# Kernel optimization log

Measured on AMD Instinct MI355X. Metric: run time of the kernel, lower is better.

## Reference

```python
import jax, jax.numpy as jnp
import numpy as np

L = 4          # GAT_LAYERS
HEADS = 4      # N_HEADS
H = 64         # transformer hidden dim
DH = H // HEADS
FIN = 32       # NODE_EMBED_SIZE
A = 15         # gats.num_actions (readout size)
OBS = 1500     # flattened obs dim
HS = 512       # hidden_size (policy FC)
NOUT = 15      # num_outputs
VH = 128       # VALUE_HIDDENS
B = 128        # batch of graphs
N = 1000       # nodes per map graph
TOT = B * N
DEG = 4
E = TOT * DEG


def _lin(key, fan_in, shape):
    return jax.random.normal(key, shape, jnp.float32) * (1.0 / np.sqrt(fan_in))


def setup_inputs() -> dict:
    key = jax.random.key(0)
    ks = jax.random.split(key, 30)
    node_feats = jax.random.normal(ks[0], (TOT, FIN), jnp.float32)
    obs = jax.random.normal(ks[1], (B, OBS), jnp.float32)
    # batched-graph edges: endpoints stay within each graph (DGL batch semantics)
    off = (jnp.arange(B) * N)[:, None]
    edge_src = (jax.random.randint(ks[2], (B, N * DEG), 0, N) + off).reshape(-1).astype(jnp.int32)
    edge_dst = (jax.random.randint(ks[3], (B, N * DEG), 0, N) + off).reshape(-1).astype(jnp.int32)
    agent_nodes = (jax.random.randint(ks[4], (B,), 0, N) + jnp.arange(B) * N).astype(jnp.int32)
    p = {
        'W_in': _lin(ks[5], FIN, (FIN, H)),
        'Wq': _lin(ks[6], H, (L, H, H)), 'Wk': _lin(ks[7], H, (L, H, H)),
        'Wv': _lin(ks[8], H, (L, H, H)), 'Wo': _lin(ks[9], H, (L, H, H)),
        'ln1_g': jnp.ones((L, H), jnp.float32), 'ln1_b': jnp.zeros((L, H), jnp.float32),
        'W1': _lin(ks[10], H, (L, H, 2 * H)), 'b1': jnp.zeros((L, 2 * H), jnp.float32),
        'W2': _lin(ks[11], 2 * H, (L, 2 * H, H)), 'b2': jnp.zeros((L, H), jnp.float32),
        'ln2_g': jnp.ones((L, H), jnp.float32), 'ln2_b': jnp.zeros((L, H), jnp.float32),
        'Wr': _lin(ks[12], H, (H, A)), 'br': jnp.zeros((A,), jnp.float32),
        'Wp1': _lin(ks[13], A + OBS, (A + OBS, HS)), 'bp1': jnp.zeros((HS,), jnp.float32),
        'Wp2': _lin(ks[14], HS, (HS, HS)), 'bp2': jnp.zeros((HS,), jnp.float32),
        'Wlog': _lin(ks[15], HS, (HS, NOUT)), 'blog': jnp.zeros((NOUT,), jnp.float32),
        'Wv1': _lin(ks[16], OBS, (OBS, VH)), 'bv1': jnp.zeros((VH,), jnp.float32),
        'Wv2': _lin(ks[17], VH, (VH, VH)), 'bv2': jnp.zeros((VH,), jnp.float32),
        'Wvo': _lin(ks[18], VH, (VH, 1)), 'bvo': jnp.zeros((1,), jnp.float32),
    }
    return dict(node_feats=node_feats, obs=obs, edge_src=edge_src, edge_dst=edge_dst,
                agent_nodes=agent_nodes, **p)


def _layernorm(x, g, b):
    m = x.mean(-1, keepdims=True)
    v = ((x - m) ** 2).mean(-1, keepdims=True)
    return (x - m) * jax.lax.rsqrt(v + 1e-5) * g + b


def reference(node_feats, obs, edge_src, edge_dst, agent_nodes, W_in, Wq, Wk, Wv, Wo,
              ln1_g, ln1_b, W1, b1, W2, b2, ln2_g, ln2_b, Wr, br,
              Wp1, bp1, Wp2, bp2, Wlog, blog, Wv1, bv1, Wv2, bv2, Wvo, bvo):
    n = node_feats.shape[0]
    x = node_feats @ W_in                                   # [n, H]
    inv_sqrt_dh = np.float32(1.0 / np.sqrt(DH))
    for l in range(L):
        q = (x @ Wq[l]).reshape(n, HEADS, DH)
        k = (x @ Wk[l]).reshape(n, HEADS, DH)
        v = (x @ Wv[l]).reshape(n, HEADS, DH)
        # per-edge attention scores, softmax over incoming edges of each dst node
        s = jnp.sum(q[edge_dst] * k[edge_src], axis=-1) * inv_sqrt_dh   # [E, HEADS]
        m = jax.ops.segment_max(s, edge_dst, num_segments=n)            # [n, HEADS]
        w = jnp.exp(s - m[edge_dst])
        denom = jax.ops.segment_sum(w, edge_dst, num_segments=n)        # [n, HEADS]
        agg = jax.ops.segment_sum(w[:, :, None] * v[edge_src], edge_dst, num_segments=n)
        attn = (agg / (denom[:, :, None] + 1e-9)).reshape(n, H) @ Wo[l]
        x = _layernorm(x + attn, ln1_g[l], ln1_b[l])
        h = jax.nn.relu(x @ W1[l] + b1[l]) @ W2[l] + b2[l]
        x = _layernorm(x + h, ln2_g[l], ln2_b[l])
    gat_out = x[agent_nodes] @ Wr + br                      # [B, A] per-agent action features
    feat = jnp.tanh(jnp.concatenate([gat_out, obs], axis=1) @ Wp1 + bp1)
    feat = jnp.tanh(feat @ Wp2 + bp2)
    logits = feat @ Wlog + blog                             # [B, NOUT]
    vh = jnp.tanh(obs @ Wv1 + bv1)
    vh = jnp.tanh(vh @ Wv2 + bv2)
    value = (vh @ Wvo + bvo)[:, 0]                          # [B]
    return logits, value
```

## Files before the change

### kernel.cpp

```cpp
#include <hip/hip_runtime.h>
#include <hip/hip_bf16.h>
#include <cstdint>
#include <cstddef>

#define DEV static __device__ __forceinline__

constexpr int GRAPHS = 128;
constexpr int NPG    = 1000;
constexpr int EPG    = 4000;
constexpr int TOTN   = GRAPHS * NPG;
constexpr int TOTE   = GRAPHS * EPG;
constexpr int HD     = 64;
constexpr int OBSD   = 1500;
constexpr int AD     = 15;

typedef __attribute__((ext_vector_type(8))) short bf16x8;
typedef __attribute__((ext_vector_type(4))) float f32x4;

DEV unsigned short f2b(float f){
  unsigned u = __float_as_uint(f);
  return (unsigned short)((u + 0x7fffu + ((u >> 16) & 1u)) >> 16);
}
DEV float b2f(unsigned short s){ return __uint_as_float((unsigned)s << 16); }

DEV void fma4(float4& a, float s, const float4 w){
  a.x = fmaf(s, w.x, a.x); a.y = fmaf(s, w.y, a.y);
  a.z = fmaf(s, w.z, a.z); a.w = fmaf(s, w.w, a.w);
}

DEV ushort4 pack4(float4 v){
  ushort4 r; r.x=f2b(v.x); r.y=f2b(v.y); r.z=f2b(v.z); r.w=f2b(v.w); return r;
}

__global__ __launch_bounds__(256) void k_wprep(const float* __restrict__ Wq,
    const float* __restrict__ Wk, const float* __restrict__ Wv,
    const float* __restrict__ Wo, const float* __restrict__ W1,
    const float* __restrict__ W2, unsigned short* __restrict__ wpack){
  int e = blockIdx.x*256 + threadIdx.x;
  int l = e >> 15;
  int r = e & 32767;
  float val;
  if (r < 12288){
    int c = r >> 6, k = r & 63;
    val = (c < 64)  ? Wq[l*4096 + k*64 + c]
        : (c < 128) ? Wk[l*4096 + k*64 + (c-64)]
                    : Wv[l*4096 + k*64 + (c-128)];
  } else if (r < 16384){
    int i = r - 12288; int c = i >> 6, k = i & 63;
    val = Wo[l*4096 + k*64 + c];
  } else if (r < 24576){
    int i = r - 16384; int c = i >> 6, k = i & 63;
    val = W1[l*8192 + k*128 + c];
  } else {
    int i = r - 24576; int c = i >> 7, k = i & 127;
    val = W2[l*8192 + k*64 + c];
  }
  wpack[e] = f2b(val);
}

__global__ __launch_bounds__(256) void k_zero(int* __restrict__ cnt){
  cnt[blockIdx.x*256 + threadIdx.x] = 0;
}

__global__ __launch_bounds__(256) void k_hist(const int* __restrict__ edst,
                                              int* __restrict__ cnt){
  int e = blockIdx.x*256 + threadIdx.x;
  atomicAdd(&cnt[edst[e]], 1);
}

__global__ __launch_bounds__(1024) void k_scan(const int* __restrict__ cnt,
    int* __restrict__ rstart, int* __restrict__ cursor){
  __shared__ int s[1024];
  const int g = blockIdx.x, tid = threadIdx.x;
  int v = (tid < NPG) ? cnt[g*NPG + tid] : 0;
  s[tid] = v;
  __syncthreads();
  #pragma unroll
  for (int off=1; off<1024; off<<=1){
    int t = (tid >= off) ? s[tid-off] : 0;
    __syncthreads();
    s[tid] += t;
    __syncthreads();
  }
  if (tid < NPG){
    int r = g*EPG + (s[tid] - v);
    rstart[g*NPG+tid] = r;
    cursor[g*NPG+tid] = r;
  }
}

__global__ __launch_bounds__(256) void k_scatter(const int* __restrict__ esrc,
    const int* __restrict__ edst, int* __restrict__ cursor,
    int* __restrict__ esorted){
  int e = blockIdx.x*256 + threadIdx.x;
  int pos = atomicAdd(&cursor[edst[e]], 1);
  esorted[pos] = esrc[e];
}

__global__ __launch_bounds__(256) void k_in(const float* __restrict__ nf,
                                            const float* __restrict__ Win,
                                            unsigned short* __restrict__ xb){
  __shared__ float  s_nf[256*36];
  __shared__ float4 s_w[512];
  const int tid = threadIdx.x;
  const int node0 = blockIdx.x * 256;
  const float4* W4 = (const float4*)Win;
  s_w[tid] = W4[tid]; s_w[tid+256] = W4[tid+256];
  const float4* nf4 = (const float4*)nf;
  float4* snf4 = (float4*)s_nf;
  #pragma unroll
  for (int r=0;r<8;r++){
    int i = tid + 256*r; int n = i>>3, k4 = i&7;
    snf4[n*9 + k4] = nf4[(size_t)(node0+n)*8 + k4];
  }
  __syncthreads();
  const int ng = tid>>2, cg = tid&3;
  float4 acc[4][4];
  #pragma unroll
  for (int i=0;i<4;i++){ acc[i][0]=make_float4(0,0,0,0); acc[i][1]=make_float4(0,0,0,0);
                         acc[i][2]=make_float4(0,0,0,0); acc[i][3]=make_float4(0,0,0,0); }
  #pragma unroll 4
  for (int k=0;k<32;k++){
    float nv[4];
    #pragma unroll
    for (int i=0;i<4;i++) nv[i] = s_nf[(ng + 64*i)*36 + k];
    float4 w[4];
    #pragma unroll
    for (int j=0;j<4;j++) w[j] = s_w[k*16 + cg*4 + j];
    #pragma unroll
    for (int i=0;i<4;i++){
      #pragma unroll
      for (int j=0;j<4;j++) fma4(acc[i][j], nv[i], w[j]);
    }
  }
  ushort4* xb4 = (ushort4*)xb;
  #pragma unroll
  for (int i=0;i<4;i++){
    size_t nidx = (size_t)(node0 + ng + 64*i) * 16;
    #pragma unroll
    for (int j=0;j<4;j++) xb4[nidx + cg*4 + j] = pack4(acc[i][j]);
  }
}

__global__ __launch_bounds__(256) void k_qkv_m(const unsigned short* __restrict__ xb,
    const unsigned short* __restrict__ wqkvT,
    unsigned short* __restrict__ qkv){
  __shared__ short s_w[192*72];
  __shared__ short s_st[4][16*104];
  const int tid = threadIdx.x;
  const int node0 = blockIdx.x * 256;
  {
    const unsigned* src = (const unsigned*)wqkvT;
    unsigned* dst = (unsigned*)s_w;
    #pragma unroll
    for (int r=0;r<24;r++){
      int j = tid + 256*r;
      int c = j >> 5, kk = j & 31;
      dst[c*36 + kk] = src[j];
    }
  }
  __syncthreads();
  const int lane = tid & 63, wave = tid >> 6;
  const int m = lane & 15, quad = lane >> 4;
  const int rowbase = node0 + wave*64;
  bf16x8 af[4][2];
  #pragma unroll
  for (int rt=0;rt<4;rt++){
    const unsigned short* xp = xb + (size_t)(rowbase + rt*16 + m)*64 + quad*8;
    af[rt][0] = *(const bf16x8*)xp;
    af[rt][1] = *(const bf16x8*)(xp + 32);
  }
  short* st = s_st[wave];
  #pragma unroll
  for (int rt=0;rt<4;rt++){
    #pragma unroll
    for (int half=0; half<2; half++){
      #pragma unroll
      for (int c6=0;c6<6;c6++){
        int ct = half*6 + c6;
        bf16x8 b0 = *(const bf16x8*)&s_w[(ct*16+m)*72 + quad*8];
        bf16x8 b1 = *(const bf16x8*)&s_w[(ct*16+m)*72 + 32 + quad*8];
        f32x4 acc = {0.f,0.f,0.f,0.f};
        acc = __builtin_amdgcn_mfma_f32_16x16x32_bf16(af[rt][0], b0, acc, 0,0,0);
        acc = __builtin_amdgcn_mfma_f32_16x16x32_bf16(af[rt][1], b1, acc, 0,0,0);
        #pragma unroll
        for (int i=0;i<4;i++)
          st[(quad*4+i)*104 + c6*16 + m] = (short)f2b(acc[i]);
      }
      #pragma unroll
      for (int j=0;j<3;j++){
        int flat = (j*64 + lane)*8;
        int r = flat / 96, c = flat % 96;
        bf16x8 v = *(const bf16x8*)&st[r*104 + c];
        *(bf16x8*)(qkv + (size_t)(rowbase + rt*16 + r)*192 + half*96 + c) = v;
      }
    }
  }
}

__global__ __launch_bounds__(256) void k_edge2(const unsigned short* __restrict__ qkv,
    const int* __restrict__ rstart, const int* __restrict__ cnt,
    const int* __restrict__ esorted, unsigned short* __restrict__ attn_in){
  const int tid = threadIdx.x;
  const int wb = (blockIdx.x & 7)*1000 + (blockIdx.x >> 3);
  const int lane = tid & 63;
  const int sub  = lane >> 4;
  const int dg   = lane & 15;
  const int wave = tid >> 6;
  const int node = wb*16 + wave*4 + sub;
  ushort4 qu = *(const ushort4*)(qkv + (size_t)node*192 + dg*4);
  float q0 = b2f(qu.x), q1 = b2f(qu.y), q2 = b2f(qu.z), q3 = b2f(qu.w);
  const int rs = rstart[node];
  const int n  = cnt[node];
  const int nn = min(n, 16);
  int myidx = (dg < nn) ? esorted[rs + dg] : node;
  const int lbase = lane & 48;
  float a0=0.f, a1=0.f, a2=0.f, a3=0.f, den=0.f;
  ushort4 kA, vA, kB, vB;
  if (nn > 0){
    int s0 = __shfl(myidx, lbase);
    kA = *(const ushort4*)(qkv + (size_t)s0*192 + 64 + dg*4);
    vA = *(const ushort4*)(qkv + (size_t)s0*192 + 128 + dg*4);
  }
  if (nn > 1){
    int s1 = __shfl(myidx, lbase + 1);
    kB = *(const ushort4*)(qkv + (size_t)s1*192 + 64 + dg*4);
    vB = *(const ushort4*)(qkv + (size_t)s1*192 + 128 + dg*4);
  }
  for (int i=0;i<nn;i++){
    ushort4 ck = kA, cv = vA;
    kA = kB; vA = vB;
    if (i+2 < nn){
      int s2 = __shfl(myidx, lbase + i + 2);
      kB = *(const ushort4*)(qkv + (size_t)s2*192 + 64 + dg*4);
      vB = *(const ushort4*)(qkv + (size_t)s2*192 + 128 + dg*4);
    }
    float p = q0*b2f(ck.x) + q1*b2f(ck.y) + q2*b2f(ck.z) + q3*b2f(ck.w);
    p += __shfl_xor(p, 1);
    p += __shfl_xor(p, 2);
    float w = __expf(p * 0.25f);
    den += w;
    a0 = fmaf(w, b2f(cv.x), a0);
    a1 = fmaf(w, b2f(cv.y), a1);
    a2 = fmaf(w, b2f(cv.z), a2);
    a3 = fmaf(w, b2f(cv.w), a3);
  }
  for (int i=16;i<n;i++){
    int src = esorted[rs + i];
    ushort4 ku = *(const ushort4*)(qkv + (size_t)src*192 + 64 + dg*4);
    ushort4 vu = *(const ushort4*)(qkv + (size_t)src*192 + 128 + dg*4);
    float p = q0*b2f(ku.x) + q1*b2f(ku.y) + q2*b2f(ku.z) + q3*b2f(ku.w);
    p += __shfl_xor(p, 1);
    p += __shfl_xor(p, 2);
    float w = __expf(p * 0.25f);
    den += w;
    a0 = fmaf(w, b2f(vu.x), a0);
    a1 = fmaf(w, b2f(vu.y), a1);
    a2 = fmaf(w, b2f(vu.z), a2);
    a3 = fmaf(w, b2f(vu.w), a3);
  }
  float inv = 1.0f/(den + 1e-9f);
  ushort4 o;
  o.x = f2b(a0*inv); o.y = f2b(a1*inv); o.z = f2b(a2*inv); o.w = f2b(a3*inv);
  ((ushort4*)attn_in)[(size_t)node*16 + dg] = o;
}

__global__ __launch_bounds__(256) void k_attn_ffn(
    const unsigned short* __restrict__ attn_in,
    unsigned short* __restrict__ xb,
    const unsigned short* __restrict__ woT,
    const unsigned short* __restrict__ w1T, const float* __restrict__ b1_l,
    const unsigned short* __restrict__ w2T, const float* __restrict__ b2_l,
    const float* __restrict__ l1g, const float* __restrict__ l1b,
    const float* __restrict__ l2g, const float* __restrict__ l2b,
    const unsigned short* __restrict__ wqkvT,
    unsigned short* __restrict__ qkv){
  __shared__ short s_w1[128*72];
  __shared__ short s_w2[64*136];
  __shared__ short s_st[4][16*136];
  const int tid = threadIdx.x;
  const int node0 = blockIdx.x*256;
  {
    const unsigned* src = (const unsigned*)w1T;
    unsigned* dst = (unsigned*)s_w1;
    #pragma unroll
    for (int r=0;r<16;r++){
      int j = tid + 256*r;
      int c = j >> 5, kk = j & 31;
      dst[c*36 + kk] = src[j];
    }
  }
  {
    const unsigned* src = (const unsigned*)w2T;
    unsigned* dst = (unsigned*)s_w2;
    #pragma unroll
    for (int r=0;r<16;r++){
      int j = tid + 256*r;
      int c = j >> 6, kk = j & 63;
      dst[c*68 + kk] = src[j];
    }
  }
  const int lane = tid&63, wave = tid>>6;
  const int m = lane&15, quad = lane>>4;
  const int rowbase = node0 + wave*64;
  bf16x8 wo[4][2];
  #pragma unroll
  for (int ct=0;ct<4;ct++){
    wo[ct][0] = *(const bf16x8*)&woT[(ct*16+m)*64 + quad*8];
    wo[ct][1] = *(const bf16x8*)&woT[(ct*16+m)*64 + 32 + quad*8];
  }
  float g1[4], bb1[4], g2[4], bb2[4], b2v[4];
  #pragma unroll
  for (int ct=0;ct<4;ct++){
    g1[ct]=l1g[ct*16+m]; bb1[ct]=l1b[ct*16+m];
    g2[ct]=l2g[ct*16+m]; bb2[ct]=l2b[ct*16+m];
    b2v[ct]=b2_l[ct*16+m];
  }
  float b1v[8];
  #pragma unroll
  for (int ct=0;ct<8;ct++) b1v[ct]=b1_l[ct*16+m];
  bf16x8 af[4][2];
  #pragma unroll
  for (int rt=0;rt<4;rt++){
    const unsigned short* ap = attn_in + (size_t)(rowbase + rt*16 + m)*64 + quad*8;
    af[rt][0] = *(const bf16x8*)ap;
    af[rt][1] = *(const bf16x8*)(ap + 32);
  }
  __syncthreads();
  short* st = s_st[wave];
  #pragma unroll
  for (int rt=0;rt<4;rt++){
    f32x4 acc[4];
    #pragma unroll
    for (int ct=0;ct<4;ct++){
      f32x4 z = {0.f,0.f,0.f,0.f};
      z = __builtin_amdgcn_mfma_f32_16x16x32_bf16(af[rt][0], wo[ct][0], z, 0,0,0);
      z = __builtin_amdgcn_mfma_f32_16x16x32_bf16(af[rt][1], wo[ct][1], z, 0,0,0);
      acc[ct] = z;
    }
    float x1v[4][4];
    #pragma unroll
    for (int i=0;i<4;i++){
      size_t row = (size_t)(rowbase + rt*16 + quad*4 + i)*64;
      float v0 = acc[0][i] + b2f(xb[row + m]);
      float v1 = acc[1][i] + b2f(xb[row + 16 + m]);
      float v2 = acc[2][i] + b2f(xb[row + 32 + m]);
      float v3 = acc[3][i] + b2f(xb[row + 48 + m]);
      float sm = v0+v1+v2+v3;
      float sq = v0*v0+v1*v1+v2*v2+v3*v3;
      #pragma unroll
      for (int mk=1; mk<16; mk<<=1){ sm += __shfl_xor(sm, mk); sq += __shfl_xor(sq, mk); }
      float mean = sm*0.015625f;
      float var  = sq*0.015625f - mean*mean;
      float rs   = rsqrtf(var + 1e-5f);
      x1v[i][0] = (v0-mean)*rs*g1[0]+bb1[0];
      x1v[i][1] = (v1-mean)*rs*g1[1]+bb1[1];
      x1v[i][2] = (v2-mean)*rs*g1[2]+bb1[2];
      x1v[i][3] = (v3-mean)*rs*g1[3]+bb1[3];
      int rl = quad*4 + i;
      st[rl*136 + m]      = (short)f2b(x1v[i][0]);
      st[rl*136 + 16 + m] = (short)f2b(x1v[i][1]);
      st[rl*136 + 32 + m] = (short)f2b(x1v[i][2]);
      st[rl*136 + 48 + m] = (short)f2b(x1v[i][3]);
    }
    bf16x8 x10 = *(const bf16x8*)&st[m*136 + quad*8];
    bf16x8 x11 = *(const bf16x8*)&st[m*136 + 32 + quad*8];
    #pragma unroll
    for (int ct=0;ct<8;ct++){
      bf16x8 b0 = *(const bf16x8*)&s_w1[(ct*16+m)*72 + quad*8];
      bf16x8 b1 = *(const bf16x8*)&s_w1[(ct*16+m)*72 + 32 + quad*8];
      f32x4 z = {0.f,0.f,0.f,0.f};
      z = __builtin_amdgcn_mfma_f32_16x16x32_bf16(x10, b0, z, 0,0,0);
      z = __builtin_amdgcn_mfma_f32_16x16x32_bf16(x11, b1, z, 0,0,0);
      #pragma unroll
      for (int i=0;i<4;i++)
        st[(quad*4+i)*136 + ct*16 + m] = (short)f2b(fmaxf(z[i]+b1v[ct], 0.f));
    }
    bf16x8 h0 = *(const bf16x8*)&st[m*136 + quad*8];
    bf16x8 h1 = *(const bf16x8*)&st[m*136 + 32 + quad*8];
    bf16x8 h2 = *(const bf16x8*)&st[m*136 + 64 + quad*8];
    bf16x8 h3 = *(const bf16x8*)&st[m*136 + 96 + quad*8];
    f32x4 acc2[4];
    #pragma unroll
    for (int ct=0;ct<4;ct++){
      f32x4 z = {0.f,0.f,0.f,0.f};
      z = __builtin_amdgcn_mfma_f32_16x16x32_bf16(h0, *(const bf16x8*)&s_w2[(ct*16+m)*136 + quad*8],      z, 0,0,0);
      z = __builtin_amdgcn_mfma_f32_16x16x32_bf16(h1, *(const bf16x8*)&s_w2[(ct*16+m)*136 + 32 + quad*8], z, 0,0,0);
      z = __builtin_amdgcn_mfma_f32_16x16x32_bf16(h2, *(const bf16x8*)&s_w2[(ct*16+m)*136 + 64 + quad*8], z, 0,0,0);
      z = __builtin_amdgcn_mfma_f32_16x16x32_bf16(h3, *(const bf16x8*)&s_w2[(ct*16+m)*136 + 96 + quad*8], z, 0,0,0);
      acc2[ct] = z;
    }
    #pragma unroll
    for (int i=0;i<4;i++){
      float v0 = acc2[0][i] + b2v[0] + x1v[i][0];
      float v1 = acc2[1][i] + b2v[1] + x1v[i][1];
      float v2 = acc2[2][i] + b2v[2] + x1v[i][2];
      float v3 = acc2[3][i] + b2v[3] + x1v[i][3];
      float sm = v0+v1+v2+v3;
      float sq = v0*v0+v1*v1+v2*v2+v3*v3;
      #pragma unroll
      for (int mk=1; mk<16; mk<<=1){ sm += __shfl_xor(sm, mk); sq += __shfl_xor(sq, mk); }
      float mean = sm*0.015625f;
      float var  = sq*0.015625f - mean*mean;
      float rs   = rsqrtf(var + 1e-5f);
      int rl = quad*4 + i;
      st[rl*136 + m]      = (short)f2b((v0-mean)*rs*g2[0]+bb2[0]);
      st[rl*136 + 16 + m] = (short)f2b((v1-mean)*rs*g2[1]+bb2[1]);
      st[rl*136 + 32 + m] = (short)f2b((v2-mean)*rs*g2[2]+bb2[2]);
      st[rl*136 + 48 + m] = (short)f2b((v3-mean)*rs*g2[3]+bb2[3]);
    }
    #pragma unroll
    for (int j=0;j<2;j++){
      int flat = (j*64 + lane)*8;
      int r = flat >> 6, c = flat & 63;
      bf16x8 v = *(const bf16x8*)&st[r*136 + c];
      *(bf16x8*)(xb + (size_t)(rowbase + rt*16 + r)*64 + c) = v;
    }
    if (wqkvT){
      bf16x8 x20 = *(const bf16x8*)&st[m*136 + quad*8];
      bf16x8 x21 = *(const bf16x8*)&st[m*136 + 32 + quad*8];
      #pragma unroll
      for (int half=0; half<2; half++){
        #pragma unroll
        for (int c6=0;c6<6;c6++){
          int ct = half*6 + c6;
          bf16x8 b0 = *(const bf16x8*)&wqkvT[(ct*16+m)*64 + quad*8];
          bf16x8 b1 = *(const bf16x8*)&wqkvT[(ct*16+m)*64 + 32 + quad*8];
          f32x4 z = {0.f,0.f,0.f,0.f};
          z = __builtin_amdgcn_mfma_f32_16x16x32_bf16(x20, b0, z, 0,0,0);
          z = __builtin_amdgcn_mfma_f32_16x16x32_bf16(x21, b1, z, 0,0,0);
          #pragma unroll
          for (int i=0;i<4;i++)
            st[(quad*4+i)*136 + c6*16 + m] = (short)f2b(z[i]);
        }
        #pragma unroll
        for (int j=0;j<3;j++){
          int flat = (j*64 + lane)*8;
          int r = flat / 96, c = flat % 96;
          bf16x8 v = *(const bf16x8*)&st[r*136 + c];
          *(bf16x8*)(qkv + (size_t)(rowbase + rt*16 + r)*192 + half*96 + c) = v;
        }
      }
    }
  }
}

__global__ __launch_bounds__(512) void k_fc1(const unsigned short* __restrict__ xb,
    const float* __restrict__ obs, const int* __restrict__ agents,
    const float* __restrict__ Wr, const float* __restrict__ br,
    const float* __restrict__ Wp1, float* __restrict__ part1){
  constexpr int ROWS=2, COLS=256, CH=384, K=1515, N=512;
  const int chunk = 379;
  __shared__ float s_a[ROWS*CH];
  const int tid = threadIdx.x;
  const int ct = blockIdx.x, rg = blockIdx.y, ks = blockIdx.z;
  const int k0 = ks * chunk;
  const int len = min(K - k0, chunk);
  const int row0 = rg * ROWS;
  #pragma unroll
  for (int rr=0; rr<ROWS; rr++)
    for (int i=tid; i<len; i+=512){
      int k = k0 + i;
      if (k >= AD) s_a[rr*CH + i] = obs[(size_t)(row0+rr)*OBSD + (k-AD)];
    }
  if (ks==0 && tid < ROWS*AD){
    int rr = tid/AD, c = tid%AD;
    int b = row0 + rr;
    const unsigned short* xa = xb + (size_t)agents[b]*HD;
    float a = br[c];
    #pragma unroll 8
    for (int k=0;k<HD;k++) a = fmaf(b2f(xa[k]), Wr[k*AD + c], a);
    s_a[rr*CH + c] = a;
  }
  __syncthreads();
  const int r = tid / COLS, c = tid % COLS;
  const float* wp = Wp1 + (size_t)k0*N + ct*COLS + c;
  const float* ap = s_a + r*CH;
  float acc = 0.f;
  #pragma unroll 8
  for (int k=0;k<len;k++) acc = fmaf(ap[k], wp[(size_t)k*N], acc);
  part1[((size_t)ks*128 + row0 + r)*N + ct*COLS + c] = acc;
}

__global__ __launch_bounds__(512) void k_fc2(const float* __restrict__ part1,
    const float* __restrict__ bp1, const float* __restrict__ Wp2,
    float* __restrict__ part2){
  constexpr int ROWS=2, COLS=256, CH=256, N=512;
  __shared__ float s_a[ROWS*CH];
  const int tid = threadIdx.x;
  const int ct = blockIdx.x, rg = blockIdx.y, ks = blockIdx.z;
  const int k0 = ks * CH;
  const int row0 = rg * ROWS;
  #pragma unroll
  for (int rr=0; rr<ROWS; rr++)
    for (int i=tid; i<CH; i+=512){
      int k = k0 + i;
      float s = bp1[k];
      #pragma unroll
      for (int j=0;j<4;j++) s += part1[((size_t)j*128 + row0+rr)*512 + k];
      s_a[rr*CH + i] = tanhf(s);
    }
  __syncthreads();
  const int r = tid / COLS, c = tid % COLS;
  const float* wp = Wp2 + (size_t)k0*N + ct*COLS + c;
  const float* ap = s_a + r*CH;
  float acc = 0.f;
  #pragma unroll 8
  for (int k=0;k<CH;k++) acc = fmaf(ap[k], wp[(size_t)k*N], acc);
  part2[((size_t)ks*128 + row0 + r)*N + ct*COLS + c] = acc;
}

__global__ __launch_bounds__(256) void k_logits(const float* __restrict__ part2,
    const float* __restrict__ bp2, const float* __restrict__ Wlog,
    const float* __restrict__ blog, float* __restrict__ out){
  __shared__ float s_f[512];
  __shared__ float s_p[16*AD];
  const int b = blockIdx.x, tid = threadIdx.x;
  for (int i=tid;i<512;i+=256){
    float s = bp2[i] + part2[(size_t)b*512 + i] + part2[(size_t)(128+b)*512 + i];
    s_f[i] = tanhf(s);
  }
  __syncthreads();
  if (tid < 240){
    int c = tid % AD, kc = tid / AD;
    float a = 0.f;
    #pragma unroll 8
    for (int j=0;j<32;j++){ int k = kc*32 + j; a = fmaf(s_f[k], Wlog[k*AD + c], a); }
    s_p[tid] = a;
  }
  __syncthreads();
  if (tid < AD){
    float a = blog[tid];
    #pragma unroll
    for (int kc=0;kc<16;kc++) a += s_p[kc*AD + tid];
    out[(size_t)b*AD + tid] = a;
  }
}

template<int ROWS, int COLS, int CH, int KS, int N>
__global__ __launch_bounds__(ROWS*COLS) void k_gemm_part(
    const float* __restrict__ A, int lda, int K,
    const float* __restrict__ W, float* __restrict__ part){
  constexpr int BT = ROWS*COLS;
  __shared__ float s_a[ROWS*CH];
  const int tid = threadIdx.x;
  const int ct = blockIdx.x, rg = blockIdx.y, ks = blockIdx.z;
  const int chunk = (K + KS - 1) / KS;
  const int k0 = ks * chunk;
  const int len = min(K - k0, chunk);
  const int row0 = rg * ROWS;
  #pragma unroll
  for (int rr=0; rr<ROWS; rr++)
    for (int i=tid; i<len; i+=BT)
      s_a[rr*CH + i] = A[(size_t)(row0+rr)*lda + k0 + i];
  __syncthreads();
  const int r = tid / COLS, c = tid % COLS;
  const float* wp = W + (size_t)k0*N + ct*COLS + c;
  const float* ap = s_a + r*CH;
  float acc = 0.f;
  #pragma unroll 8
  for (int k=0;k<len;k++) acc = fmaf(ap[k], wp[(size_t)k*N], acc);
  part[((size_t)ks*128 + row0 + r)*N + ct*COLS + c] = acc;
}

__global__ __launch_bounds__(128) void k_vfin(const float* __restrict__ partv,
    const float* __restrict__ bv1, const float* __restrict__ Wv2,
    const float* __restrict__ bv2, const float* __restrict__ Wvo,
    const float* __restrict__ bvo, float* __restrict__ out){
  __shared__ float s_v[128];
  __shared__ float s_r[128];
  const int b = blockIdx.x, tid = threadIdx.x;
  {
    float s = bv1[tid];
    #pragma unroll
    for (int j=0;j<8;j++) s += partv[((size_t)j*128 + b)*128 + tid];
    s_v[tid] = tanhf(s);
  }
  __syncthreads();
  float a = bv2[tid];
  #pragma unroll 8
  for (int k=0;k<128;k++) a = fmaf(s_v[k], Wv2[k*128 + tid], a);
  s_r[tid] = tanhf(a) * Wvo[tid];
  __syncthreads();
  if (tid < 64){
    float v = s_r[tid] + s_r[tid+64];
    #pragma unroll
    for (int m=32;m>=1;m>>=1) v += __shfl_xor(v, m);
    if (tid==0) out[GRAPHS*AD + b] = v + bvo[0];
  }
}

extern "C" void kernel_launch(void* const* d_in, const int* in_sizes, int n_in,
                              void* d_out, int out_size, void* d_ws, size_t ws_size,
                              hipStream_t stream) {
  (void)in_sizes; (void)n_in; (void)out_size; (void)ws_size;
  const float* nf     = (const float*)d_in[0];
  const float* obs    = (const float*)d_in[1];
  const int*   esrc   = (const int*)d_in[2];
  const int*   edst   = (const int*)d_in[3];
  const int*   agents = (const int*)d_in[4];
  const float* Win    = (const float*)d_in[5];
  const float* Wq     = (const float*)d_in[6];
  const float* Wk     = (const float*)d_in[7];
  const float* Wv     = (const float*)d_in[8];
  const float* Wo     = (const float*)d_in[9];
  const float* ln1g   = (const float*)d_in[10];
  const float* ln1b   = (const float*)d_in[11];
  const float* W1     = (const float*)d_in[12];
  const float* b1     = (const float*)d_in[13];
  const float* W2     = (const float*)d_in[14];
  const float* b2     = (const float*)d_in[15];
  const float* ln2g   = (const float*)d_in[16];
  const float* ln2b   = (const float*)d_in[17];
  const float* Wr     = (const float*)d_in[18];
  const float* br     = (const float*)d_in[19];
  const float* Wp1    = (const float*)d_in[20];
  const float* bp1    = (const float*)d_in[21];
  const float* Wp2    = (const float*)d_in[22];
  const float* bp2    = (const float*)d_in[23];
  const float* Wlog   = (const float*)d_in[24];
  const float* blog   = (const float*)d_in[25];
  const float* Wv1    = (const float*)d_in[26];
  const float* bv1    = (const float*)d_in[27];
  const float* Wv2    = (const float*)d_in[28];
  const float* bv2    = (const float*)d_in[29];
  const float* Wvo    = (const float*)d_in[30];
  const float* bvo    = (const float*)d_in[31];
  float* out = (float*)d_out;

  unsigned short* xb      = (unsigned short*)d_ws;
  unsigned short* qkv     = xb + (size_t)TOTN*HD;
  unsigned short* attn_in = qkv + (size_t)TOTN*192;
  unsigned short* wpack   = attn_in + (size_t)TOTN*HD;
  int* cnt     = (int*)(wpack + 131072);
  int* rstart  = cnt + TOTN;
  int* cursor  = rstart + TOTN;
  int* esorted = cursor + TOTN;
  float* part1 = (float*)(esorted + TOTE);
  float* part2 = part1 + 4*128*512;
  float* partv = part2 + 2*128*512;

  k_wprep  <<<512, 256, 0, stream>>>(Wq, Wk, Wv, Wo, W1, W2, wpack);
  k_zero   <<<TOTN/256, 256, 0, stream>>>(cnt);
  k_hist   <<<TOTE/256, 256, 0, stream>>>(edst, cnt);
  k_scan   <<<GRAPHS, 1024, 0, stream>>>(cnt, rstart, cursor);
  k_scatter<<<TOTE/256, 256, 0, stream>>>(esrc, edst, cursor, esorted);

  k_in<<<TOTN/256, 256, 0, stream>>>(nf, Win, xb);
  k_qkv_m<<<TOTN/256, 256, 0, stream>>>(xb, wpack, qkv);
  for (int l=0; l<4; l++){
    const unsigned short* wl = wpack + l*32768;
    const unsigned short* wqkv_next = (l<3) ? (wpack + (l+1)*32768) : nullptr;
    k_edge2   <<<TOTN/16, 256, 0, stream>>>(qkv, rstart, cnt, esorted, attn_in);
    k_attn_ffn<<<TOTN/256, 256, 0, stream>>>(attn_in, xb,
                                             wl + 12288,
                                             wl + 16384, b1 + l*128,
                                             wl + 24576, b2 + l*64,
                                             ln1g + l*64, ln1b + l*64,
                                             ln2g + l*64, ln2b + l*64,
                                             wqkv_next, qkv);
  }
  k_fc1   <<<dim3(2,64,4), 512, 0, stream>>>(xb, obs, agents, Wr, br, Wp1, part1);
  k_fc2   <<<dim3(2,64,2), 512, 0, stream>>>(part1, bp1, Wp2, part2);
  k_logits<<<GRAPHS, 256, 0, stream>>>(part2, bp2, Wlog, blog, out);
  k_gemm_part<4,128,192,8,128><<<dim3(1,32,8), 512, 0, stream>>>(obs, 1500, 1500, Wv1, partv);
  k_vfin  <<<GRAPHS, 128, 0, stream>>>(partv, bv1, Wv2, bv2, Wvo, bvo, out);
}
```

Before: 483.4 us.

## Shrink attn-FFN blocks to one wave and read FFN weights from global

Result: slower. 658.8 us (+36.3%).

```diff
diff --git a/kernel.cpp b/kernel.cpp
--- a/kernel.cpp
+++ b/kernel.cpp
@@ -265,7 +265,7 @@
   ((ushort4*)attn_in)[(size_t)node*16 + dg] = o;
 }
 
-__global__ __launch_bounds__(256) void k_attn_ffn(
+__global__ __launch_bounds__(64, 4) void k_attn_ffn(
     const unsigned short* __restrict__ attn_in,
     unsigned short* __restrict__ xb,
     const unsigned short* __restrict__ woT,
@@ -275,34 +275,10 @@
     const float* __restrict__ l2g, const float* __restrict__ l2b,
     const unsigned short* __restrict__ wqkvT,
     unsigned short* __restrict__ qkv){
-  __shared__ short s_w1[128*72];
-  __shared__ short s_w2[64*136];
-  __shared__ short s_st[4][16*136];
-  const int tid = threadIdx.x;
-  const int node0 = blockIdx.x*256;
-  {
-    const unsigned* src = (const unsigned*)w1T;
-    unsigned* dst = (unsigned*)s_w1;
-    #pragma unroll
-    for (int r=0;r<16;r++){
-      int j = tid + 256*r;
-      int c = j >> 5, kk = j & 31;
-      dst[c*36 + kk] = src[j];
-    }
-  }
-  {
-    const unsigned* src = (const unsigned*)w2T;
-    unsigned* dst = (unsigned*)s_w2;
-    #pragma unroll
-    for (int r=0;r<16;r++){
-      int j = tid + 256*r;
-      int c = j >> 6, kk = j & 63;
-      dst[c*68 + kk] = src[j];
-    }
-  }
-  const int lane = tid&63, wave = tid>>6;
+  __shared__ short st[16*136];
+  const int lane = threadIdx.x;
   const int m = lane&15, quad = lane>>4;
-  const int rowbase = node0 + wave*64;
+  const int rowbase = blockIdx.x*64;
   bf16x8 wo[4][2];
   #pragma unroll
   for (int ct=0;ct<4;ct++){
@@ -326,8 +302,6 @@
     af[rt][0] = *(const bf16x8*)ap;
     af[rt][1] = *(const bf16x8*)(ap + 32);
   }
-  __syncthreads();
-  short* st = s_st[wave];
   #pragma unroll
   for (int rt=0;rt<4;rt++){
     f32x4 acc[4];
@@ -367,8 +341,8 @@
     bf16x8 x11 = *(const bf16x8*)&st[m*136 + 32 + quad*8];
     #pragma unroll
     for (int ct=0;ct<8;ct++){
-      bf16x8 b0 = *(const bf16x8*)&s_w1[(ct*16+m)*72 + quad*8];
-      bf16x8 b1 = *(const bf16x8*)&s_w1[(ct*16+m)*72 + 32 + quad*8];
+      bf16x8 b0 = *(const bf16x8*)&w1T[(ct*16+m)*64 + quad*8];
+      bf16x8 b1 = *(const bf16x8*)&w1T[(ct*16+m)*64 + 32 + quad*8];
       f32x4 z = {0.f,0.f,0.f,0.f};
       z = __builtin_amdgcn_mfma_f32_16x16x32_bf16(x10, b0, z, 0,0,0);
       z = __builtin_amdgcn_mfma_f32_16x16x32_bf16(x11, b1, z, 0,0,0);
@@ -384,10 +358,10 @@
     #pragma unroll
     for (int ct=0;ct<4;ct++){
       f32x4 z = {0.f,0.f,0.f,0.f};
-      z = __builtin_amdgcn_mfma_f32_16x16x32_bf16(h0, *(const bf16x8*)&s_w2[(ct*16+m)*136 + quad*8],      z, 0,0,0);
-      z = __builtin_amdgcn_mfma_f32_16x16x32_bf16(h1, *(const bf16x8*)&s_w2[(ct*16+m)*136 + 32 + quad*8], z, 0,0,0);
-      z = __builtin_amdgcn_mfma_f32_16x16x32_bf16(h2, *(const bf16x8*)&s_w2[(ct*16+m)*136 + 64 + quad*8], z, 0,0,0);
-      z = __builtin_amdgcn_mfma_f32_16x16x32_bf16(h3, *(const bf16x8*)&s_w2[(ct*16+m)*136 + 96 + quad*8], z, 0,0,0);
+      z = __builtin_amdgcn_mfma_f32_16x16x32_bf16(h0, *(const bf16x8*)&w2T[(ct*16+m)*128 + quad*8],      z, 0,0,0);
+      z = __builtin_amdgcn_mfma_f32_16x16x32_bf16(h1, *(const bf16x8*)&w2T[(ct*16+m)*128 + 32 + quad*8], z, 0,0,0);
+      z = __builtin_amdgcn_mfma_f32_16x16x32_bf16(h2, *(const bf16x8*)&w2T[(ct*16+m)*128 + 64 + quad*8], z, 0,0,0);
+      z = __builtin_amdgcn_mfma_f32_16x16x32_bf16(h3, *(const bf16x8*)&w2T[(ct*16+m)*128 + 96 + quad*8], z, 0,0,0);
       acc2[ct] = z;
     }
     #pragma unroll
@@ -652,13 +626,13 @@
     const unsigned short* wl = wpack + l*32768;
     const unsigned short* wqkv_next = (l<3) ? (wpack + (l+1)*32768) : nullptr;
     k_edge2   <<<TOTN/16, 256, 0, stream>>>(qkv, rstart, cnt, esorted, attn_in);
-    k_attn_ffn<<<TOTN/256, 256, 0, stream>>>(attn_in, xb,
-                                             wl + 12288,
-                                             wl + 16384, b1 + l*128,
-                                             wl + 24576, b2 + l*64,
-                                             ln1g + l*64, ln1b + l*64,
-                                             ln2g + l*64, ln2b + l*64,
-                                             wqkv_next, qkv);
+    k_attn_ffn<<<TOTN/64, 64, 0, stream>>>(attn_in, xb,
+                                           wl + 12288,
+                                           wl + 16384, b1 + l*128,
+                                           wl + 24576, b2 + l*64,
+                                           ln1g + l*64, ln1b + l*64,
+                                           ln2g + l*64, ln2b + l*64,
+                                           wqkv_next, qkv);
   }
   k_fc1   <<<dim3(2,64,4), 512, 0, stream>>>(xb, obs, agents, Wr, br, Wp1, part1);
   k_fc2   <<<dim3(2,64,2), 512, 0, stream>>>(part1, bp1, Wp2, part2);
```
